# Performance work log

Measured on AMD Instinct MI355X. Metric: run time of the kernel, lower is better.

Reference implementation:

```python
import jax, jax.numpy as jnp
import numpy as np
from jax import lax

N = 5000
C = 81  # num_classes including background at index 0
BG_OFFSET = 1


def _iou_matrix(b):
    # b: [N,4] as x1,y1,x2,y2 -> pairwise IoU [N,N]
    x1, y1, x2, y2 = b[:, 0], b[:, 1], b[:, 2], b[:, 3]
    area = (x2 - x1) * (y2 - y1)  # [N]
    ix1 = jnp.maximum(x1[:, None], x1[None, :])
    iy1 = jnp.maximum(y1[:, None], y1[None, :])
    ix2 = jnp.minimum(x2[:, None], x2[None, :])
    iy2 = jnp.minimum(y2[:, None], y2[None, :])
    iw = jnp.maximum(ix2 - ix1, 0.0)
    ih = jnp.maximum(iy2 - iy1, 0.0)
    inter = iw * ih
    return inter / (area[:, None] + area[None, :] - inter)


def setup_inputs() -> dict:
    key = jax.random.key(0)
    k1, k2, k3 = jax.random.split(key, 3)
    # valid boxes: x1<x2, y1<y2 on a ~1024px canvas, size ~up to 256px
    xy1 = jax.random.uniform(k1, (N, 2), dtype=jnp.float32) * 1024.0
    wh = jax.random.uniform(k2, (N, 2), dtype=jnp.float32) * 256.0 + 1.0
    bboxes = jnp.concatenate([xy1, xy1 + wh], axis=1)  # [N,4]
    scores = jax.random.uniform(k3, (N, C), dtype=jnp.float32)  # [N,C]
    return {
        "bboxes": bboxes,
        "scores": scores,
        "conf_thresh": 0.6,
        "nms_thresh": 0.5,
        "max_instances": 300,
    }


def _multiclass_nms(bboxes, scores, conf_thresh, nms_thresh, max_instances):
    n = bboxes.shape[0]
    neg_inf = jnp.finfo(scores.dtype).min
    iou = _iou_matrix(bboxes)  # [N,N]

    def nms_one_class(score_c):  # score_c: [N]
        valid = score_c > conf_thresh
        masked = jnp.where(valid, score_c, neg_inf)
        order = jnp.argsort(masked)[::-1]  # descending score

        def step(suppressed, idx):
            keep = valid[idx] & ~suppressed[idx]
            new_sup = jnp.where(keep, suppressed | (iou[idx] > nms_thresh), suppressed)
            return new_sup, keep

        _, keeps = lax.scan(step, jnp.zeros((n,), bool), order)
        # scatter keep flags back to original box order
        return jnp.zeros((n,), bool).at[order].set(keeps)

    fg_scores = scores[:, BG_OFFSET:].T  # [C-1, N]
    keep = jax.vmap(nms_one_class)(fg_scores)  # [C-1, N]

    # global top-k over all (class, box) kept detections, sorted by score desc
    flat = jnp.where(keep, fg_scores, neg_inf).reshape(-1)  # [(C-1)*N]
    top_scores, top_idx = lax.top_k(flat, max_instances)
    cls = top_idx // n + BG_OFFSET  # [K]
    box = top_idx % n  # [K]
    valid_out = top_scores > neg_inf / 2

    sel_score = scores[box, cls]  # differentiable gather
    preds = jnp.concatenate([bboxes[box], sel_score[:, None]], axis=1)  # [K,5]
    preds = jnp.where(valid_out[:, None], preds, 0.0)
    labels = jnp.where(valid_out, cls, -1)
    return preds, labels


def reference(bboxes, scores, conf_thresh, nms_thresh, max_instances):
    return _multiclass_nms(bboxes, scores, conf_thresh, nms_thresh, max_instances)
```

## Files before the change

kernel.cpp:

```cpp
#include <hip/hip_runtime.h>

typedef unsigned long long u64;
typedef unsigned int u32;
typedef unsigned short u16;

#define MSORT 4096
#define TPB1  1024
#define TPBF  1024
#define BOXCAP 3648
#define KCAP  3072
#define RSLOT_W 10
#define KPC   300
#define SELCAP 1024
#define PREFR 64
#define TBOX  128

#define WG_SCOPE __HIP_MEMORY_SCOPE_WORKGROUP

__device__ __forceinline__ float boxArea(float4 b) {
    return __fmul_rn(__fsub_rn(b.z, b.x), __fsub_rn(b.w, b.y));
}

template<bool GE>
__device__ __forceinline__ bool iou_gt(float4 a, float area_a, float4 b, float area_b, double B) {
    float ix1 = fmaxf(a.x, b.x), iy1 = fmaxf(a.y, b.y);
    float ix2 = fminf(a.z, b.z), iy2 = fminf(a.w, b.w);
    float iw  = fmaxf(__fsub_rn(ix2, ix1), 0.0f);
    float ih  = fmaxf(__fsub_rn(iy2, iy1), 0.0f);
    float inter = __fmul_rn(iw, ih);
    float uni   = __fsub_rn(__fadd_rn(area_a, area_b), inter);
    return GE ? ((double)inter >= B * (double)uni) : ((double)inter > B * (double)uni);
}

__device__ __forceinline__ int scoreBin(u32 bits) {
    int b = (int)(bits >> 12) - 0x3F000;
    return b < 0 ? 0 : (b > 2047 ? 2047 : b);
}

__device__ __forceinline__ void bstar_wave0(
    const u32* __restrict__ hist, int target, int tid,
    int* __restrict__ outBs, int* __restrict__ outTot)
{
    if (tid < 64) {
        int s = 0;
        #pragma unroll
        for (int b = 0; b < 32; b++)
            s += (int)hist[(tid << 5) + ((b + tid) & 31)];
        #pragma unroll
        for (int d = 1; d < 64; d <<= 1) {
            int v = __shfl_down(s, d, 64);
            if (tid + d < 64) s += v;
        }
        u64 bal = __ballot(s >= target);
        int ch  = bal ? (63 - __builtin_clzll(bal)) : -1;
        int tot = __shfl(s, 0, 64);
        int bs  = 0;
        if (ch >= 0) {
            int accAbove = (ch < 63) ? __shfl(s, ch + 1, 64) : 0;
            int h = (tid < 32) ? (int)hist[(ch << 5) + tid] : 0;
            #pragma unroll
            for (int d = 1; d < 32; d <<= 1) {
                int v = __shfl_down(h, d, 64);
                if (tid + d < 32) h += v;
            }
            u64 bal2 = __ballot((tid < 32) && (accAbove + h >= target));
            bs = (ch << 5) + (63 - __builtin_clzll(bal2));
        }
        if (tid == 0) { *outBs = bs; if (outTot) *outTot = tot; }
    }
}

__global__ __launch_bounds__(1024) void transpose_kernel(
    const float* __restrict__ scores, int N, int C,
    float* __restrict__ scoresT, u32* __restrict__ gHist)
{
    __shared__ float tile[TBOX * 81];
    const int tid = threadIdx.x;
    const int b0  = blockIdx.x * TBOX;
    const int nb  = (N - b0 < TBOX) ? (N - b0) : TBOX;
    const int tot = nb * C;
    for (int e = tid; e < tot; e += 1024)
        tile[e] = scores[(size_t)b0 * C + e];
    __syncthreads();
    if (nb == TBOX) {
        const int wtot = C << 7;
        for (int o = tid; o < wtot; o += 1024) {
            int cls = o >> 7, j = o & (TBOX - 1);
            scoresT[(size_t)cls * N + b0 + j] = tile[j * C + cls];
        }
    } else {
        const int wtot = C * nb;
        for (int o = tid; o < wtot; o += 1024) {
            int cls = o / nb, j = o - cls * nb;
            scoresT[(size_t)cls * N + b0 + j] = tile[j * C + cls];
        }
    }
    if (blockIdx.x == 0)
        for (int h = tid; h < 2048; h += 1024) gHist[h] = 0;
}

template<bool GE>
__device__ __forceinline__ int prefix_nms_w0(
    const float* __restrict__ bboxes, const u64* __restrict__ sorted,
    int R, double B, int tid, int c, int N, u64* __restrict__ gkept_c,
    u32* __restrict__ gHist)
{
    u64 key = (tid < R) ? sorted[tid] : 0;
    float4 bx = make_float4(0.f, 0.f, 0.f, 0.f);
    if (tid < R) bx = ((const float4*)bboxes)[(u32)key];
    float ar = boxArea(bx);
    u64 supB = (R >= 64) ? 0ull : (~0ull << R);
    int nk = 0;
    int i = -1;
    for (;;) {
        u64 mask = (i >= 63) ? 0ull : (~0ull << (i + 1));
        u64 alive = ~supB & mask;
        if (!alive) break;
        i = (int)__builtin_ctzll(alive);
        float4 bi;
        bi.x = __shfl(bx.x, i, 64); bi.y = __shfl(bx.y, i, 64);
        bi.z = __shfl(bx.z, i, 64); bi.w = __shfl(bx.w, i, 64);
        float ai = boxArea(bi);
        if (tid == 0) {
            u64 ki = sorted[i];
            u32 flat = (u32)c * (u32)N + (u32)ki;
            gkept_c[nk] = (ki & 0xFFFFFFFF00000000ull) | (u32)(~flat);
        }
        nk++;
        bool sup = (tid > i) && iou_gt<GE>(bi, ai, bx, ar, B);
        supB |= __ballot(sup);
    }
    if (tid < R && !((supB >> tid) & 1ull))
        atomicAdd(&gHist[scoreBin((u32)(key >> 32))], 1u);
    return nk;
}

__global__ __launch_bounds__(TPB1, 1) void nms_select_kernel(
    const float* __restrict__ bboxes, const float* __restrict__ scoresT,
    const float* __restrict__ conf_ptr, const float* __restrict__ nms_ptr,
    int N, u64* __restrict__ gkept,
    u32* __restrict__ gK, u32* __restrict__ g65, u32* __restrict__ gPre,
    u32* __restrict__ gHist)
{
    __shared__ u64 keys[KCAP];
    __shared__ u32 hist[2048];
    __shared__ u64 keybuf[256];
    __shared__ u64 sorted[66];
    __shared__ int cntS, ncollS, bstarS, nkS;

    const int tid  = threadIdx.x;
    const int lane = tid & 63;
    const int c    = blockIdx.x;
    const int cls  = c + 1;
    const float conf = *conf_ptr;
    const float nmsT = *nms_ptr;

    for (int b = tid; b < 2048; b += TPB1) hist[b] = 0;
    if (tid < 66) sorted[tid] = 0;
    if (tid == 0) { cntS = 0; ncollS = 0; nkS = 0; }
    __syncthreads();

    const float* rowT = scoresT + (size_t)cls * N;
    const float4* rowT4 = (const float4*)rowT;
    const int N4 = N >> 2;
    for (int i4 = tid; i4 < N4; i4 += TPB1) {
        float4 s4 = rowT4[i4];
        #pragma unroll
        for (int j = 0; j < 4; j++) {
            float s = (j == 0) ? s4.x : (j == 1) ? s4.y : (j == 2) ? s4.z : s4.w;
            bool pass = (s > conf);
            u64 m = __ballot(pass);
            if (m) {
                int leader = (int)__builtin_ctzll(m);
                int base = 0;
                if (lane == leader) base = atomicAdd(&cntS, __popcll(m));
                base = __shfl(base, leader, 64);
                if (pass) {
                    int p = base + (int)__popcll(m & ((1ull << lane) - 1ull));
                    if (p < KCAP)
                        keys[p] = ((u64)__float_as_uint(s) << 32) | (u32)((i4 << 2) + j);
                    atomicAdd(&hist[scoreBin(__float_as_uint(s))], 1u);
                }
            }
        }
    }
    for (int i = (N4 << 2) + tid; i < N; i += TPB1) {
        float s = rowT[i];
        if (s > conf) {
            int p = atomicAdd(&cntS, 1);
            if (p < KCAP) keys[p] = ((u64)__float_as_uint(s) << 32) | (u32)i;
            atomicAdd(&hist[scoreBin(__float_as_uint(s))], 1u);
        }
    }
    __syncthreads();
    const int K = cntS;
    const bool preOv = (K > KCAP);
    const int target = K < (PREFR + 1) ? K : (PREFR + 1);

    bstar_wave0(hist, target, tid, &bstarS, nullptr);
    __syncthreads();
    const u32 tbits = (bstarS == 0) ? 0u : (((u32)bstarS + 0x3F000u) << 12);

    const int KL = K < KCAP ? K : KCAP;
    for (int p = tid; p < KL; p += TPB1) {
        u64 k = keys[p];
        if ((u32)(k >> 32) >= tbits) {
            int pos = atomicAdd(&ncollS, 1);
            if (pos < 256) keybuf[pos] = k;
        }
    }
    __syncthreads();
    const int ncoll = ncollS;
    const bool pre = preOv || (ncoll > 256);
    for (int p = ncoll + tid; p < 256; p += TPB1) keybuf[p] = 0;
    __syncthreads();

    u64* gkept_c = gkept + (size_t)c * KPC;
    if (!pre) {
        if (tid < 256) {
            u64 my = keybuf[tid];
            int rank = 0;
            for (int j = 0; j < 256; j++) rank += (keybuf[j] > my);
            if (my && rank < PREFR + 1) sorted[rank] = my;
        }
        __syncthreads();
        const u32 tb = __float_as_uint(nmsT);
        const float Tn = __uint_as_float(tb + 1u);
        const double B = ((double)nmsT + (double)Tn) * 0.5;
        const bool geCmp = (((tb + 1u) & 1u) == 0u);
        if (tid < 64) {
            int R = ncoll < PREFR ? ncoll : PREFR;
            int nk = geCmp ? prefix_nms_w0<true >(bboxes, sorted, R, B, tid, c, N, gkept_c, gHist)
                           : prefix_nms_w0<false>(bboxes, sorted, R, B, tid, c, N, gkept_c, gHist);
            if (tid == 0) nkS = nk;
        }
        __syncthreads();
        for (int p = nkS + tid; p < KPC; p += TPB1) gkept_c[p] = 0;
    } else {
        for (int p = tid; p < KPC; p += TPB1) gkept_c[p] = 0;
    }
    if (tid == 0) {
        gK[c]   = (u32)K;
        g65[c]  = pre ? 0xFFFFFFFFu : ((ncoll >= PREFR + 1) ? (u32)(sorted[PREFR] >> 32) : 0u);
        gPre[c] = pre ? 1u : 0u;
    }
}

__global__ __launch_bounds__(1024) void nms_theta_kernel(
    const u32* __restrict__ gHist, const u32* __restrict__ gK,
    const u32* __restrict__ g65, const u32* __restrict__ gPre,
    int nc, int Mout, u32* __restrict__ gCtl)
{
    __shared__ u32 hist[2048];
    __shared__ int thBs, thTot;
    const int tid = threadIdx.x;
    for (int b = tid; b < 2048; b += 1024) hist[b] = gHist[b];
    __syncthreads();
    bstar_wave0(hist, Mout, tid, &thBs, &thTot);
    __syncthreads();
    u32 theta = 0u;
    if (thTot >= Mout && thBs > 0) theta = (((u32)thBs + 0x3F000u) << 12);
    if (tid == 0) gCtl[0] = theta;
    for (int c2 = tid; c2 < nc; c2 += 1024) {
        u32 need = gPre[c2];
        if (gK[c2] > PREFR && g65[c2] >= theta) need = 1u;
        gCtl[1 + c2] = need;
    }
}

template<bool GE>
__device__ __forceinline__ u64 sweep_own(
    float4 bi, float area_i, const float4 (&breg)[RSLOT_W],
    const float (&areaj)[RSLOT_W], const float4* __restrict__ boxesLds,
    int base, int nslots, int lane, double B)
{
    u64 ns = 0;
    #pragma unroll
    for (int t = 0; t < RSLOT_W; t++)
        ns |= ((u64)iou_gt<GE>(bi, area_i, breg[t], areaj[t], B)) << (base + t);
    for (int t = RSLOT_W; t < nslots; t++) {
        float4 bj = boxesLds[((base + t) << 6) | lane];
        ns |= ((u64)iou_gt<GE>(bi, area_i, bj, boxArea(bj), B)) << (base + t);
    }
    return ns;
}

template<bool GE>
__device__ __forceinline__ int greedy_full(
    const float4* __restrict__ boxesLds, u16* __restrict__ keptR,
    float4* __restrict__ pubBox, u32* __restrict__ ctl,
    const u32* __restrict__ gsi_c, const float* __restrict__ rowT,
    u32 thetaBits,
    int K, int smax, double B, int lane, int wave)
{
    const int SW   = (smax + 3) >> 2;
    const int base = (wave * SW < smax) ? wave * SW : smax;
    const int end  = (base + SW < smax) ? base + SW : smax;
    const int nslots = end - base;

    float4 breg[RSLOT_W];
    float  areaj[RSLOT_W];
    #pragma unroll
    for (int t = 0; t < RSLOT_W; t++) {
        float4 b = boxesLds[((base + t) << 6) | lane];
        breg[t] = b;
        areaj[t] = boxArea(b);
    }

    u64 sup;
    {
        int t = (lane < K) ? ((K - lane + 63) >> 6) : 0;
        sup = (t >= 64) ? 0ull : (~0ull << t);
    }

    u32 seen = 0;
    if (wave != 0) {
        for (;;) {
            u32 d  = __hip_atomic_load(&ctl[2], __ATOMIC_ACQUIRE, WG_SCOPE);
            u32 cn = __hip_atomic_load(&ctl[0], __ATOMIC_ACQUIRE, WG_SCOPE);
            bool prog = (seen < cn);
            while (seen < cn) {
                float4 bi = pubBox[seen]; seen++;
                sup |= sweep_own<GE>(bi, boxArea(bi), breg, areaj, boxesLds, base, nslots, lane, B);
            }
            if (d) return -1;
            u32 aw = __hip_atomic_load(&ctl[1], __ATOMIC_ACQUIRE, WG_SCOPE);
            if (aw == (u32)wave) {
                u32 cn2 = __hip_atomic_load(&ctl[0], __ATOMIC_ACQUIRE, WG_SCOPE);
                while (seen < cn2) {
                    float4 bi = pubBox[seen]; seen++;
                    sup |= sweep_own<GE>(bi, boxArea(bi), breg, areaj, boxesLds, base, nslots, lane, B);
                }
                break;
            }
            if (!prog) __builtin_amdgcn_s_sleep(1);
        }
    }

    u32 nk = seen;
    const u32 seen0 = seen;
    int scur = base - 1;
    float4 bcur = make_float4(0.f, 0.f, 0.f, 0.f);
    float  acur = 0.f;
    int js = base << 6;

    for (;;) {
        int s = js >> 6;
        while (s > scur) {
            scur++;
            if (scur < end) {
                bcur = boxesLds[(scur << 6) | lane];
                acur = boxArea(bcur);
                u64 bit = 0;
                for (u32 k = seen0; k < nk; k++) {
                    float4 bk = pubBox[k];
                    bit |= ((u64)iou_gt<GE>(bk, boxArea(bk), bcur, acur, B));
                }
                sup |= bit << scur;
            }
        }
        if (scur >= end) {
            if (wave == 3) {
                if (lane == 0) __hip_atomic_store(&ctl[2], 1u, __ATOMIC_RELEASE, WG_SCOPE);
                return (int)nk;
            }
            if (lane == 0) __hip_atomic_store(&ctl[1], (u32)(wave + 1), __ATOMIC_RELEASE, WG_SCOPE);
            return -1;
        }
        u64 bal = __ballot((int)(((~sup) >> scur) & 1ull)) & (~0ull << (js & 63));
        if (bal == 0) { js = (scur + 1) << 6; continue; }
        int i = (scur << 6) + (int)__builtin_ctzll(bal);

        if (thetaBits) {
            u32 idx = gsi_c[i];
            float sc = rowT[idx];
            if (__float_as_uint(sc) < thetaBits) {
                if (lane == 0) __hip_atomic_store(&ctl[2], 1u, __ATOMIC_RELEASE, WG_SCOPE);
                return (int)nk;
            }
        }
        float4 bi = boxesLds[i];
        if (lane == 0) { pubBox[nk] = bi; keptR[nk] = (u16)i; }
        nk++;
        if (nk >= KPC) {
            if (lane == 0) {
                __hip_atomic_store(&ctl[0], nk, __ATOMIC_RELEASE, WG_SCOPE);
                __hip_atomic_store(&ctl[2], 1u, __ATOMIC_RELEASE, WG_SCOPE);
            }
            return (int)nk;
        }
        if (lane == 0) __hip_atomic_store(&ctl[0], nk, __ATOMIC_RELEASE, WG_SCOPE);
        sup |= ((u64)iou_gt<GE>(bi, boxArea(bi), bcur, acur, B)) << scur;
        js = i + 1;
    }
}

__global__ __launch_bounds__(TPBF, 1) void nms_full_kernel(
    const float* __restrict__ bboxes, const float* __restrict__ scoresT,
    const float* __restrict__ conf_ptr, const float* __restrict__ nms_ptr,
    int N, const u32* __restrict__ gCtl,
    u32* __restrict__ gsi, u64* __restrict__ gkept)
{
    const int c = blockIdx.x;
    if (gCtl[1 + c] == 0u) return;

    __shared__ __align__(16) char smem[63856];
    u64*    sortbuf  = (u64*)smem;
    float4* boxesLds = (float4*)smem;
    u16*    keptR    = (u16*)(smem + 58368);
    u32*    ctl      = (u32*)(smem + 58976);
    float4* pubBox   = (float4*)(smem + 58992);
    __shared__ int cntS;

    const int tid  = threadIdx.x;
    const int lane = tid & 63;
    const int cls = c + 1;
    const float conf = *conf_ptr;
    const float nmsT = *nms_ptr;
    const u32 thetaBits = gCtl[0];

    if (tid == 0) cntS = 0;
    __syncthreads();
    const float* rowT = scoresT + (size_t)cls * N;
    const float4* rowT4 = (const float4*)rowT;
    const int N4 = N >> 2;
    for (int i4 = tid; i4 < N4; i4 += TPBF) {
        float4 s4 = rowT4[i4];
        #pragma unroll
        for (int j = 0; j < 4; j++) {
            float s = (j == 0) ? s4.x : (j == 1) ? s4.y : (j == 2) ? s4.z : s4.w;
            bool pass = (s > conf);
            u64 m = __ballot(pass);
            if (m) {
                int leader = (int)__builtin_ctzll(m);
                int base = 0;
                if (lane == leader) base = atomicAdd(&cntS, __popcll(m));
                base = __shfl(base, leader, 64);
                if (pass) {
                    int p = base + (int)__popcll(m & ((1ull << lane) - 1ull));
                    if (p < MSORT)
                        sortbuf[p] = ((u64)__float_as_uint(s) << 32) | (u32)((i4 << 2) + j);
                }
            }
        }
    }
    for (int i = (N4 << 2) + tid; i < N; i += TPBF) {
        float s = rowT[i];
        if (s > conf) {
            int p = atomicAdd(&cntS, 1);
            if (p < MSORT) sortbuf[p] = ((u64)__float_as_uint(s) << 32) | (u32)i;
        }
    }
    __syncthreads();
    int K = cntS; if (K > BOXCAP) K = BOXCAP;
    int M = 64; while (M < K) M <<= 1;
    for (int p = K + tid; p < M; p += TPBF) sortbuf[p] = 0;
    __syncthreads();
    for (int kk = 2; kk <= M; kk <<= 1) {
        for (int j = kk >> 1; j > 0; j >>= 1) {
            for (int i = tid; i < M; i += TPBF) {
                int ixj = i ^ j;
                if (ixj > i) {
                    u64 a = sortbuf[i], b = sortbuf[ixj];
                    if (((i & kk) == 0) ? (a < b) : (a > b)) { sortbuf[i] = b; sortbuf[ixj] = a; }
                }
            }
            __syncthreads();
        }
    }
    u32 myIdx[MSORT / TPBF];
    #pragma unroll
    for (int t = 0; t < MSORT / TPBF; t++) myIdx[t] = (u32)sortbuf[t * TPBF + tid];
    __syncthreads();
    u32* gsi_c = gsi + (size_t)c * BOXCAP;
    #pragma unroll
    for (int t = 0; t < MSORT / TPBF; t++) {
        int r = t * TPBF + tid;
        if (r < K) {
            u32 idx = myIdx[t];
            gsi_c[r] = idx;
            boxesLds[r] = ((const float4*)bboxes)[idx];
        }
    }
    if (tid == 0) { ctl[0] = 0; ctl[1] = 0; ctl[2] = 0; }
    __syncthreads();
    if (tid >= 256) return;

    const int wave = tid >> 6;
    const u32 tb = __float_as_uint(nmsT);
    const float Tn = __uint_as_float(tb + 1u);
    const double B = ((double)nmsT + (double)Tn) * 0.5;
    const bool geCmp = (((tb + 1u) & 1u) == 0u);
    const int smax = (K + 63) >> 6;

    int ret = geCmp ? greedy_full<true >(boxesLds, keptR, pubBox, ctl, gsi_c, rowT, thetaBits, K, smax, B, lane, wave)
                    : greedy_full<false>(boxesLds, keptR, pubBox, ctl, gsi_c, rowT, thetaBits, K, smax, B, lane, wave);
    if (ret >= 0) {
        int kept = ret; if (kept > KPC) kept = KPC;
        u64* gkept_c = gkept + (size_t)c * KPC;
        for (int p = lane; p < kept; p += 64) {
            int rank = keptR[p];
            u32 idx = gsi_c[rank];
            float sc = rowT[idx];
            u32 flat = (u32)c * (u32)N + idx;
            gkept_c[p] = ((u64)__float_as_uint(sc) << 32) | (u32)(~flat);
        }
        for (int p = kept + lane; p < KPC; p += 64) gkept_c[p] = 0;
    }
}

__global__ __launch_bounds__(1024) void nms_topk_kernel(
    const float* __restrict__ bboxes, const u64* __restrict__ gkept,
    int N, int nc, int Mout, float* __restrict__ out)
{
    __shared__ u32 hist[2048];
    __shared__ int selCount;
    __shared__ int bstarS;
    __shared__ u64 sel[SELCAP];

    const int tid = threadIdx.x;
    const int total = nc * KPC;

    for (int b = tid; b < 2048; b += 1024) hist[b] = 0;
    if (tid == 0) selCount = 0;
    __syncthreads();

    for (int t = tid; t < total; t += 1024) {
        u64 k = gkept[t];
        if (k) atomicAdd(&hist[scoreBin((u32)(k >> 32))], 1u);
    }
    __syncthreads();

    bstar_wave0(hist, Mout, tid, &bstarS, nullptr);
    __syncthreads();
    const int bstar = bstarS;

    for (int t = tid; t < total; t += 1024) {
        u64 k = gkept[t];
        if (k && scoreBin((u32)(k >> 32)) >= bstar) {
            int p = atomicAdd(&selCount, 1);
            if (p < SELCAP) sel[p] = k;
        }
    }
    __syncthreads();
    int cnt = selCount; if (cnt > SELCAP) cnt = SELCAP;
    int SM = 512; while (SM < cnt) SM <<= 1;
    for (int p = cnt + tid; p < SM; p += 1024) sel[p] = 0;
    __syncthreads();

    for (int kk = 2; kk <= SM; kk <<= 1) {
        for (int j = kk >> 1; j > 0; j >>= 1) {
            for (int i = tid; i < SM; i += 1024) {
                int ixj = i ^ j;
                if (ixj > i) {
                    u64 a = sel[i], b = sel[ixj];
                    if (((i & kk) == 0) ? (a < b) : (a > b)) { sel[i] = b; sel[ixj] = a; }
                }
            }
            __syncthreads();
        }
    }

    for (int t = tid; t < Mout; t += 1024) {
        u64 k = (t < SM) ? sel[t] : 0;
        float px1 = 0.f, py1 = 0.f, px2 = 0.f, py2 = 0.f, ps = 0.f, plab = -1.0f;
        if (k) {
            float s  = __uint_as_float((u32)(k >> 32));
            u32 flat = ~((u32)k);
            int cc   = (int)(flat / (u32)N);
            int box  = (int)(flat - (u32)cc * (u32)N);
            float4 bb = ((const float4*)bboxes)[box];
            px1 = bb.x; py1 = bb.y; px2 = bb.z; py2 = bb.w; ps = s;
            plab = (float)(cc + 1);
        }
        out[t * 5 + 0] = px1;
        out[t * 5 + 1] = py1;
        out[t * 5 + 2] = px2;
        out[t * 5 + 3] = py2;
        out[t * 5 + 4] = ps;
        out[Mout * 5 + t] = plab;
    }
}

extern "C" void kernel_launch(void* const* d_in, const int* in_sizes, int n_in,
                              void* d_out, int out_size, void* d_ws, size_t ws_size,
                              hipStream_t stream) {
    const float* bboxes = (const float*)d_in[0];
    const float* scores = (const float*)d_in[1];
    const float* conf   = (const float*)d_in[2];
    const float* nmsT   = (const float*)d_in[3];

    const int N    = in_sizes[0] / 4;
    const int C    = in_sizes[1] / N;
    const int nc   = C - 1;
    const int Mout = out_size / 6;

    char* wsb = (char*)d_ws;
    size_t off = 0;
    float* scoresT = (float*)(wsb + off); off += ((size_t)C * N * sizeof(float) + 255) & ~(size_t)255;
    u32* gsi   = (u32*)(wsb + off); off += (size_t)nc * BOXCAP * sizeof(u32);
    u64* gkept = (u64*)(wsb + off); off += (size_t)nc * KPC * sizeof(u64);
    u32* gK    = (u32*)(wsb + off); off += (size_t)((nc + 1) & ~1) * sizeof(u32);
    u32* g65   = (u32*)(wsb + off); off += (size_t)((nc + 1) & ~1) * sizeof(u32);
    u32* gPre  = (u32*)(wsb + off); off += (size_t)((nc + 1) & ~1) * sizeof(u32);
    u32* gCtl  = (u32*)(wsb + off); off += (size_t)((1 + nc + 1) & ~1) * sizeof(u32);
    u32* gHist = (u32*)(wsb + off); off += 2048 * sizeof(u32);

    const int ntile = (N + TBOX - 1) / TBOX;
    transpose_kernel<<<ntile, 1024, 0, stream>>>(scores, N, C, scoresT, gHist);
    nms_select_kernel<<<nc, TPB1, 0, stream>>>(bboxes, scoresT, conf, nmsT, N,
                                               gkept, gK, g65, gPre, gHist);
    nms_theta_kernel<<<1, 1024, 0, stream>>>(gHist, gK, g65, gPre, nc, Mout, gCtl);
    nms_full_kernel<<<nc, TPBF, 0, stream>>>(bboxes, scoresT, conf, nmsT, N, gCtl, gsi, gkept);
    nms_topk_kernel<<<1, 1024, 0, stream>>>(bboxes, gkept, N, nc, Mout, (float*)d_out);
}
```

Baseline: 124.6 us.

## Fuse theta, full NMS and top-k kernels into one last-block-done kernel

Merges the single-block theta kernel, the per-class full NMS kernel and the single-block top-k kernel into one launch. Each block recomputes the theta threshold redundantly from the global histogram. Completion is counted with a device-scope atomic, and the last block to finish performs the global top-k and writes the output. This removes two kernel launches and their inter-kernel gaps. In exchange, every block does extra histogram work, and the final top-k runs serially on one block that must wait for all the others.

```diff
diff --git a/kernel.cpp b/kernel.cpp
--- a/kernel.cpp
+++ b/kernel.cpp
@@ -15,7 +15,8 @@
 #define PREFR 64
 #define TBOX  128
 
-#define WG_SCOPE __HIP_MEMORY_SCOPE_WORKGROUP
+#define WG_SCOPE  __HIP_MEMORY_SCOPE_WORKGROUP
+#define DEV_SCOPE __HIP_MEMORY_SCOPE_AGENT
 
 __device__ __forceinline__ float boxArea(float4 b) {
     return __fmul_rn(__fsub_rn(b.z, b.x), __fsub_rn(b.w, b.y));
@@ -96,7 +97,7 @@
         }
     }
     if (blockIdx.x == 0)
-        for (int h = tid; h < 2048; h += 1024) gHist[h] = 0;
+        for (int h = tid; h < 2052; h += 1024) gHist[h] = 0;
 }
 
 template<bool GE>
@@ -246,28 +247,6 @@
     }
 }
 
-__global__ __launch_bounds__(1024) void nms_theta_kernel(
-    const u32* __restrict__ gHist, const u32* __restrict__ gK,
-    const u32* __restrict__ g65, const u32* __restrict__ gPre,
-    int nc, int Mout, u32* __restrict__ gCtl)
-{
-    __shared__ u32 hist[2048];
-    __shared__ int thBs, thTot;
-    const int tid = threadIdx.x;
-    for (int b = tid; b < 2048; b += 1024) hist[b] = gHist[b];
-    __syncthreads();
-    bstar_wave0(hist, Mout, tid, &thBs, &thTot);
-    __syncthreads();
-    u32 theta = 0u;
-    if (thTot >= Mout && thBs > 0) theta = (((u32)thBs + 0x3F000u) << 12);
-    if (tid == 0) gCtl[0] = theta;
-    for (int c2 = tid; c2 < nc; c2 += 1024) {
-        u32 need = gPre[c2];
-        if (gK[c2] > PREFR && g65[c2] >= theta) need = 1u;
-        gCtl[1 + c2] = need;
-    }
-}
-
 template<bool GE>
 __device__ __forceinline__ u64 sweep_own(
     float4 bi, float area_i, const float4 (&breg)[RSLOT_W],
@@ -395,162 +374,179 @@
     }
 }
 
-__global__ __launch_bounds__(TPBF, 1) void nms_full_kernel(
+__global__ __launch_bounds__(TPBF, 1) void nms_finale_kernel(
     const float* __restrict__ bboxes, const float* __restrict__ scoresT,
     const float* __restrict__ conf_ptr, const float* __restrict__ nms_ptr,
-    int N, const u32* __restrict__ gCtl,
-    u32* __restrict__ gsi, u64* __restrict__ gkept)
+    int N, const u32* __restrict__ gHist,
+    const u32* __restrict__ gK, const u32* __restrict__ g65, const u32* __restrict__ gPre,
+    u32* __restrict__ gsi, u64* __restrict__ gkept,
+    int Mout, float* __restrict__ out, u32* __restrict__ gDone)
 {
-    const int c = blockIdx.x;
-    if (gCtl[1 + c] == 0u) return;
-
     __shared__ __align__(16) char smem[63856];
-    u64*    sortbuf  = (u64*)smem;
-    float4* boxesLds = (float4*)smem;
-    u16*    keptR    = (u16*)(smem + 58368);
-    u32*    ctl      = (u32*)(smem + 58976);
-    float4* pubBox   = (float4*)(smem + 58992);
-    __shared__ int cntS;
-
+    __shared__ int cntS, lastS, selCountS, bs4S, thBs, thTot;
+
+    const int c    = blockIdx.x;
     const int tid  = threadIdx.x;
     const int lane = tid & 63;
-    const int cls = c + 1;
-    const float conf = *conf_ptr;
-    const float nmsT = *nms_ptr;
-    const u32 thetaBits = gCtl[0];
-
-    if (tid == 0) cntS = 0;
-    __syncthreads();
-    const float* rowT = scoresT + (size_t)cls * N;
-    const float4* rowT4 = (const float4*)rowT;
-    const int N4 = N >> 2;
-    for (int i4 = tid; i4 < N4; i4 += TPBF) {
-        float4 s4 = rowT4[i4];
+
+    u32* histT = (u32*)smem;
+    for (int b = tid; b < 2048; b += TPBF) histT[b] = gHist[b];
+    __syncthreads();
+    bstar_wave0(histT, Mout, tid, &thBs, &thTot);
+    __syncthreads();
+    const u32 thetaBits = (thTot >= Mout && thBs > 0) ? (((u32)thBs + 0x3F000u) << 12) : 0u;
+    u32 need = gPre[c];
+    if (gK[c] > PREFR && g65[c] >= thetaBits) need = 1u;
+    __syncthreads();
+
+    if (need) {
+        u64*    sortbuf  = (u64*)smem;
+        float4* boxesLds = (float4*)smem;
+        u16*    keptR    = (u16*)(smem + 58368);
+        u32*    ctl      = (u32*)(smem + 58976);
+        float4* pubBox   = (float4*)(smem + 58992);
+
+        const int cls = c + 1;
+        const float conf = *conf_ptr;
+        const float nmsT = *nms_ptr;
+
+        if (tid == 0) cntS = 0;
+        __syncthreads();
+        const float* rowT = scoresT + (size_t)cls * N;
+        const float4* rowT4 = (const float4*)rowT;
+        const int N4 = N >> 2;
+        for (int i4 = tid; i4 < N4; i4 += TPBF) {
+            float4 s4 = rowT4[i4];
+            #pragma unroll
+            for (int j = 0; j < 4; j++) {
+                float s = (j == 0) ? s4.x : (j == 1) ? s4.y : (j == 2) ? s4.z : s4.w;
+                bool pass = (s > conf);
+                u64 m = __ballot(pass);
+                if (m) {
+                    int leader = (int)__builtin_ctzll(m);
+                    int base = 0;
+                    if (lane == leader) base = atomicAdd(&cntS, __popcll(m));
+                    base = __shfl(base, leader, 64);
+                    if (pass) {
+                        int p = base + (int)__popcll(m & ((1ull << lane) - 1ull));
+                        if (p < MSORT)
+                            sortbuf[p] = ((u64)__float_as_uint(s) << 32) | (u32)((i4 << 2) + j);
+                    }
+                }
+            }
+        }
+        for (int i = (N4 << 2) + tid; i < N; i += TPBF) {
+            float s = rowT[i];
+            if (s > conf) {
+                int p = atomicAdd(&cntS, 1);
+                if (p < MSORT) sortbuf[p] = ((u64)__float_as_uint(s) << 32) | (u32)i;
+            }
+        }
+        __syncthreads();
+        int K = cntS; if (K > BOXCAP) K = BOXCAP;
+        int M = 64; while (M < K) M <<= 1;
+        for (int p = K + tid; p < M; p += TPBF) sortbuf[p] = 0;
+        __syncthreads();
+        for (int kk = 2; kk <= M; kk <<= 1) {
+            for (int j = kk >> 1; j > 0; j >>= 1) {
+                for (int i = tid; i < M; i += TPBF) {
+                    int ixj = i ^ j;
+                    if (ixj > i) {
+                        u64 a = sortbuf[i], b = sortbuf[ixj];
+                        if (((i & kk) == 0) ? (a < b) : (a > b)) { sortbuf[i] = b; sortbuf[ixj] = a; }
+                    }
+                }
+                __syncthreads();
+            }
+        }
+        u32 myIdx[MSORT / TPBF];
         #pragma unroll
-        for (int j = 0; j < 4; j++) {
-            float s = (j == 0) ? s4.x : (j == 1) ? s4.y : (j == 2) ? s4.z : s4.w;
-            bool pass = (s > conf);
-            u64 m = __ballot(pass);
-            if (m) {
-                int leader = (int)__builtin_ctzll(m);
-                int base = 0;
-                if (lane == leader) base = atomicAdd(&cntS, __popcll(m));
-                base = __shfl(base, leader, 64);
-                if (pass) {
-                    int p = base + (int)__popcll(m & ((1ull << lane) - 1ull));
-                    if (p < MSORT)
-                        sortbuf[p] = ((u64)__float_as_uint(s) << 32) | (u32)((i4 << 2) + j);
+        for (int t = 0; t < MSORT / TPBF; t++) myIdx[t] = (u32)sortbuf[t * TPBF + tid];
+        __syncthreads();
+        u32* gsi_c = gsi + (size_t)c * BOXCAP;
+        #pragma unroll
+        for (int t = 0; t < MSORT / TPBF; t++) {
+            int r = t * TPBF + tid;
+            if (r < K) {
+                u32 idx = myIdx[t];
+                gsi_c[r] = idx;
+                boxesLds[r] = ((const float4*)bboxes)[idx];
+            }
+        }
+        if (tid == 0) { ctl[0] = 0; ctl[1] = 0; ctl[2] = 0; }
+        __syncthreads();
+
+        if (tid < 256) {
+            const int wave = tid >> 6;
+            const u32 tb = __float_as_uint(nmsT);
+            const float Tn = __uint_as_float(tb + 1u);
+            const double B = ((double)nmsT + (double)Tn) * 0.5;
+            const bool geCmp = (((tb + 1u) & 1u) == 0u);
+            const int smax = (K + 63) >> 6;
+
+            int ret = geCmp ? greedy_full<true >(boxesLds, keptR, pubBox, ctl, gsi_c, rowT, thetaBits, K, smax, B, lane, wave)
+                            : greedy_full<false>(boxesLds, keptR, pubBox, ctl, gsi_c, rowT, thetaBits, K, smax, B, lane, wave);
+            if (ret >= 0) {
+                int kept = ret; if (kept > KPC) kept = KPC;
+                u64* gkept_c = gkept + (size_t)c * KPC;
+                for (int p = lane; p < kept; p += 64) {
+                    int rank = keptR[p];
+                    u32 idx = gsi_c[rank];
+                    float sc = rowT[idx];
+                    u32 flat = (u32)c * (u32)N + idx;
+                    gkept_c[p] = ((u64)__float_as_uint(sc) << 32) | (u32)(~flat);
                 }
-            }
-        }
-    }
-    for (int i = (N4 << 2) + tid; i < N; i += TPBF) {
-        float s = rowT[i];
-        if (s > conf) {
-            int p = atomicAdd(&cntS, 1);
-            if (p < MSORT) sortbuf[p] = ((u64)__float_as_uint(s) << 32) | (u32)i;
-        }
-    }
-    __syncthreads();
-    int K = cntS; if (K > BOXCAP) K = BOXCAP;
-    int M = 64; while (M < K) M <<= 1;
-    for (int p = K + tid; p < M; p += TPBF) sortbuf[p] = 0;
-    __syncthreads();
-    for (int kk = 2; kk <= M; kk <<= 1) {
-        for (int j = kk >> 1; j > 0; j >>= 1) {
-            for (int i = tid; i < M; i += TPBF) {
-                int ixj = i ^ j;
-                if (ixj > i) {
-                    u64 a = sortbuf[i], b = sortbuf[ixj];
-                    if (((i & kk) == 0) ? (a < b) : (a > b)) { sortbuf[i] = b; sortbuf[ixj] = a; }
-                }
-            }
-            __syncthreads();
-        }
-    }
-    u32 myIdx[MSORT / TPBF];
-    #pragma unroll
-    for (int t = 0; t < MSORT / TPBF; t++) myIdx[t] = (u32)sortbuf[t * TPBF + tid];
-    __syncthreads();
-    u32* gsi_c = gsi + (size_t)c * BOXCAP;
-    #pragma unroll
-    for (int t = 0; t < MSORT / TPBF; t++) {
-        int r = t * TPBF + tid;
-        if (r < K) {
-            u32 idx = myIdx[t];
-            gsi_c[r] = idx;
-            boxesLds[r] = ((const float4*)bboxes)[idx];
-        }
-    }
-    if (tid == 0) { ctl[0] = 0; ctl[1] = 0; ctl[2] = 0; }
-    __syncthreads();
-    if (tid >= 256) return;
-
-    const int wave = tid >> 6;
-    const u32 tb = __float_as_uint(nmsT);
-    const float Tn = __uint_as_float(tb + 1u);
-    const double B = ((double)nmsT + (double)Tn) * 0.5;
-    const bool geCmp = (((tb + 1u) & 1u) == 0u);
-    const int smax = (K + 63) >> 6;
-
-    int ret = geCmp ? greedy_full<true >(boxesLds, keptR, pubBox, ctl, gsi_c, rowT, thetaBits, K, smax, B, lane, wave)
-                    : greedy_full<false>(boxesLds, keptR, pubBox, ctl, gsi_c, rowT, thetaBits, K, smax, B, lane, wave);
-    if (ret >= 0) {
-        int kept = ret; if (kept > KPC) kept = KPC;
-        u64* gkept_c = gkept + (size_t)c * KPC;
-        for (int p = lane; p < kept; p += 64) {
-            int rank = keptR[p];
-            u32 idx = gsi_c[rank];
-            float sc = rowT[idx];
-            u32 flat = (u32)c * (u32)N + idx;
-            gkept_c[p] = ((u64)__float_as_uint(sc) << 32) | (u32)(~flat);
-        }
-        for (int p = kept + lane; p < KPC; p += 64) gkept_c[p] = 0;
-    }
-}
-
-__global__ __launch_bounds__(1024) void nms_topk_kernel(
-    const float* __restrict__ bboxes, const u64* __restrict__ gkept,
-    int N, int nc, int Mout, float* __restrict__ out)
-{
-    __shared__ u32 hist[2048];
-    __shared__ int selCount;
-    __shared__ int bstarS;
-    __shared__ u64 sel[SELCAP];
-
-    const int tid = threadIdx.x;
-    const int total = nc * KPC;
-
-    for (int b = tid; b < 2048; b += 1024) hist[b] = 0;
-    if (tid == 0) selCount = 0;
-    __syncthreads();
-
-    for (int t = tid; t < total; t += 1024) {
+                for (int p = kept + lane; p < KPC; p += 64) gkept_c[p] = 0;
+            }
+        }
+    }
+
+    __syncthreads();
+    if (tid == 0) {
+        u32 v = need ? __hip_atomic_fetch_add(gDone, 1u, __ATOMIC_RELEASE, DEV_SCOPE)
+                     : __hip_atomic_fetch_add(gDone, 1u, __ATOMIC_RELAXED, DEV_SCOPE);
+        lastS = (v == (u32)(gridDim.x - 1)) ? 1 : 0;
+    }
+    __syncthreads();
+    if (!lastS) return;
+    if (tid == 0)
+        __hip_atomic_fetch_add(gDone, 0u, __ATOMIC_ACQUIRE, DEV_SCOPE);
+    __syncthreads();
+
+    u64* sel   = (u64*)smem;
+    u32* hist4 = (u32*)(smem + 8192);
+    const int total = (int)gridDim.x * KPC;
+
+    for (int b = tid; b < 2048; b += TPBF) hist4[b] = 0;
+    if (tid == 0) selCountS = 0;
+    __syncthreads();
+
+    for (int t = tid; t < total; t += TPBF) {
         u64 k = gkept[t];
-        if (k) atomicAdd(&hist[scoreBin((u32)(k >> 32))], 1u);
-    }
-    __syncthreads();
-
-    bstar_wave0(hist, Mout, tid, &bstarS, nullptr);
-    __syncthreads();
-    const int bstar = bstarS;
-
-    for (int t = tid; t < total; t += 1024) {
+        if (k) atomicAdd(&hist4[scoreBin((u32)(k >> 32))], 1u);
+    }
+    __syncthreads();
+
+    bstar_wave0(hist4, Mout, tid, &bs4S, nullptr);
+    __syncthreads();
+    const int bstar = bs4S;
+
+    for (int t = tid; t < total; t += TPBF) {
         u64 k = gkept[t];
         if (k && scoreBin((u32)(k >> 32)) >= bstar) {
-            int p = atomicAdd(&selCount, 1);
+            int p = atomicAdd(&selCountS, 1);
             if (p < SELCAP) sel[p] = k;
         }
     }
     __syncthreads();
-    int cnt = selCount; if (cnt > SELCAP) cnt = SELCAP;
+    int cnt = selCountS; if (cnt > SELCAP) cnt = SELCAP;
     int SM = 512; while (SM < cnt) SM <<= 1;
-    for (int p = cnt + tid; p < SM; p += 1024) sel[p] = 0;
+    for (int p = cnt + tid; p < SM; p += TPBF) sel[p] = 0;
     __syncthreads();
 
     for (int kk = 2; kk <= SM; kk <<= 1) {
         for (int j = kk >> 1; j > 0; j >>= 1) {
-            for (int i = tid; i < SM; i += 1024) {
+            for (int i = tid; i < SM; i += TPBF) {
                 int ixj = i ^ j;
                 if (ixj > i) {
                     u64 a = sel[i], b = sel[ixj];
@@ -561,7 +557,7 @@
         }
     }
 
-    for (int t = tid; t < Mout; t += 1024) {
+    for (int t = tid; t < Mout; t += TPBF) {
         u64 k = (t < SM) ? sel[t] : 0;
         float px1 = 0.f, py1 = 0.f, px2 = 0.f, py2 = 0.f, ps = 0.f, plab = -1.0f;
         if (k) {
@@ -603,14 +599,14 @@
     u32* gK    = (u32*)(wsb + off); off += (size_t)((nc + 1) & ~1) * sizeof(u32);
     u32* g65   = (u32*)(wsb + off); off += (size_t)((nc + 1) & ~1) * sizeof(u32);
     u32* gPre  = (u32*)(wsb + off); off += (size_t)((nc + 1) & ~1) * sizeof(u32);
-    u32* gCtl  = (u32*)(wsb + off); off += (size_t)((1 + nc + 1) & ~1) * sizeof(u32);
-    u32* gHist = (u32*)(wsb + off); off += 2048 * sizeof(u32);
+    u32* gHist = (u32*)(wsb + off); off += 2052 * sizeof(u32);
+    u32* gDone = gHist + 2048;
 
     const int ntile = (N + TBOX - 1) / TBOX;
     transpose_kernel<<<ntile, 1024, 0, stream>>>(scores, N, C, scoresT, gHist);
     nms_select_kernel<<<nc, TPB1, 0, stream>>>(bboxes, scoresT, conf, nmsT, N,
                                                gkept, gK, g65, gPre, gHist);
-    nms_theta_kernel<<<1, 1024, 0, stream>>>(gHist, gK, g65, gPre, nc, Mout, gCtl);
-    nms_full_kernel<<<nc, TPBF, 0, stream>>>(bboxes, scoresT, conf, nmsT, N, gCtl, gsi, gkept);
-    nms_topk_kernel<<<1, 1024, 0, stream>>>(bboxes, gkept, N, nc, Mout, (float*)d_out);
-}
+    nms_finale_kernel<<<nc, TPBF, 0, stream>>>(bboxes, scoresT, conf, nmsT, N,
+                                               gHist, gK, g65, gPre, gsi, gkept,
+                                               Mout, (float*)d_out, gDone);
+}
```

New measurement: 123.1 us. Within noise of the previous version (-1.1%).
